# Kernel optimization log

Hardware: AMD Instinct MI355X
Metric: run time of the kernel (lower is better)

The kernel has to match this reference:

```python
import jax, jax.numpy as jnp
import numpy as np

B, S, H = 2, 2048, 4096
NH, NKV, HD = 32, 8, 128
ROPE_THETA = 10000.0


def setup_inputs() -> dict:
    key = jax.random.key(0)
    ks = jax.random.split(key, 5)
    hidden_states = jax.random.normal(ks[0], (B, S, H), dtype=jnp.float32)
    position_ids = jnp.tile(jnp.arange(S, dtype=jnp.int64)[None, :], (B, 1))
    Wq = jax.random.normal(ks[1], (H, NH * HD), dtype=jnp.float32) * 0.02
    Wk = jax.random.normal(ks[2], (H, NKV * HD), dtype=jnp.float32) * 0.02
    Wv = jax.random.normal(ks[3], (H, NKV * HD), dtype=jnp.float32) * 0.02
    Wo = jax.random.normal(ks[4], (NH * HD, H), dtype=jnp.float32) * 0.02
    return {"hidden_states": hidden_states, "position_ids": position_ids,
            "Wq": Wq, "Wk": Wk, "Wv": Wv, "Wo": Wo}


def _rotate_half(x):
    d = x.shape[-1] // 2
    return jnp.concatenate([-x[..., d:], x[..., :d]], axis=-1)


def reference(hidden_states, position_ids, Wq, Wk, Wv, Wo):
    b, s, _ = hidden_states.shape
    # QKV projections (no bias)
    q = (hidden_states @ Wq).reshape(b, s, NH, HD).transpose(0, 2, 1, 3)   # [b,nh,s,hd]
    k = (hidden_states @ Wk).reshape(b, s, NKV, HD).transpose(0, 2, 1, 3)  # [b,nkv,s,hd]
    v = (hidden_states @ Wv).reshape(b, s, NKV, HD).transpose(0, 2, 1, 3)
    # RoPE: cos/sin from cached table == analytic computation at position_ids
    inv_freq = 1.0 / (ROPE_THETA ** (jnp.arange(0, HD, 2, dtype=jnp.float32) / HD))
    freqs = position_ids.astype(jnp.float32)[:, :, None] * inv_freq  # [b,s,hd/2]
    emb = jnp.concatenate([freqs, freqs], axis=-1)                   # [b,s,hd]
    cos = jnp.cos(emb)[:, None, :, :]  # unsqueeze_dim=1 -> [b,1,s,hd]
    sin = jnp.sin(emb)[:, None, :, :]
    q = q * cos + _rotate_half(q) * sin
    k = k * cos + _rotate_half(k) * sin
    # GQA: repeat kv heads to match query heads
    groups = NH // NKV
    k = jnp.repeat(k, groups, axis=1)
    v = jnp.repeat(v, groups, axis=1)
    # causal SDPA
    scale = 1.0 / jnp.sqrt(jnp.float32(HD))
    scores = jnp.einsum('bhqd,bhkd->bhqk', q, k) * scale
    causal = jnp.tril(jnp.ones((s, s), dtype=bool))
    scores = jnp.where(causal[None, None], scores, jnp.finfo(scores.dtype).min)
    attn = jax.nn.softmax(scores, axis=-1)
    out = jnp.einsum('bhqk,bhkd->bhqd', attn, v)
    out = out.transpose(0, 2, 1, 3).reshape(b, s, NH * HD)
    return out @ Wo
```

## Files before the change

### kernel.cpp

```cpp
#include <hip/hip_runtime.h>
#include <cstdint>
#include <cstddef>

typedef unsigned short u16;
typedef unsigned int u32;
typedef short short8 __attribute__((ext_vector_type(8)));
typedef float f32x4 __attribute__((ext_vector_type(4)));

__device__ __forceinline__ u16 f2bf(float f) {
  unsigned u = __float_as_uint(f);
  u += 0x7fffu + ((u >> 16) & 1u);
  return (u16)(u >> 16);
}
__device__ __forceinline__ float bf2f(u16 h) {
  return __uint_as_float(((unsigned)h) << 16);
}
__device__ __forceinline__ u32 pack_bf2(float lo, float hi) {
  return ((u32)f2bf(hi) << 16) | (u32)f2bf(lo);
}

typedef const __attribute__((address_space(1))) unsigned int gu32_t;
typedef __attribute__((address_space(3))) unsigned int su32_t;
__device__ __forceinline__ void gl2lds16(const void* g, void* l) {
  __builtin_amdgcn_global_load_lds((gu32_t*)g, (su32_t*)l, 16, 0, 0);
}

__device__ __forceinline__ f32x4 mfma_bf16(short8 a, short8 b, f32x4 c) {
  return __builtin_amdgcn_mfma_f32_16x16x32_bf16(a, b, c, 0, 0, 0);
}

__global__ __launch_bounds__(256) void f32_to_bf16_kernel(
    const float* __restrict__ x, u16* __restrict__ y, int n) {
  int i = (blockIdx.x * 256 + threadIdx.x) * 4;
  if (i + 3 < n) {
    float4 v = *(const float4*)(x + i);
    ushort4 o;
    o.x = f2bf(v.x); o.y = f2bf(v.y); o.z = f2bf(v.z); o.w = f2bf(v.w);
    *(ushort4*)(y + i) = o;
  }
}

__global__ __launch_bounds__(256) void transpose_w_kernel(
    const float* __restrict__ W, u16* __restrict__ Wt, int K, int N) {
  __shared__ float tile[32][33];
  int n0 = blockIdx.x * 32, k0 = blockIdx.y * 32;
  int tx = threadIdx.x, ty = threadIdx.y;
#pragma unroll
  for (int j = 0; j < 4; ++j)
    tile[ty + j * 8][tx] = W[(size_t)(k0 + ty + j * 8) * N + n0 + tx];
  __syncthreads();
#pragma unroll
  for (int j = 0; j < 4; ++j)
    Wt[(size_t)(n0 + ty + j * 8) * K + k0 + tx] = f2bf(tile[tx][ty + j * 8]);
}

template <bool BF16OUT>
__global__ __launch_bounds__(256) void gemm_bt(
    const u16* __restrict__ A, const u16* __restrict__ Bt,
    float* __restrict__ Cf, u16* __restrict__ Cb, int K, int ldc) {
  __shared__ alignas(16) u16 As[128 * 32];
  __shared__ alignas(16) u16 Bs[128 * 32];
  const int tid = threadIdx.x;
  const int w = tid >> 6, lane = tid & 63;
  const int lq = lane & 15, qd = lane >> 4;
  const int wm = w >> 1, wn = w & 1;
  const int m0 = blockIdx.y * 128, n0 = blockIdx.x * 128;
  const int r4 = lane >> 2;
  const int csw = (((lane & 3) ^ ((lane >> 3) & 3)) * 8);
  const int sa = (lq >> 1) & 3;

  f32x4 acc[4][4] = {};

  const u16* ap = A + ((size_t)(m0 + w * 16 + r4) * K + csw);
  const u16* bp = Bt + ((size_t)(n0 + w * 16 + r4) * K + csw);
  u16* asd0 = &As[(w * 16) * 32];
  u16* asd1 = &As[(64 + w * 16) * 32];
  u16* bsd0 = &Bs[(w * 16) * 32];
  u16* bsd1 = &Bs[(64 + w * 16) * 32];

  for (int k0 = 0; k0 < K; k0 += 32) {
    gl2lds16(ap + k0, asd0);
    gl2lds16(ap + (size_t)64 * K + k0, asd1);
    gl2lds16(bp + k0, bsd0);
    gl2lds16(bp + (size_t)64 * K + k0, bsd1);
    __syncthreads();
    short8 af[4], bf[4];
#pragma unroll
    for (int i = 0; i < 4; ++i)
      af[i] = *(const short8*)&As[(wm * 64 + i * 16 + lq) * 32 + (qd ^ sa) * 8];
#pragma unroll
    for (int j = 0; j < 4; ++j)
      bf[j] = *(const short8*)&Bs[(wn * 64 + j * 16 + lq) * 32 + (qd ^ sa) * 8];
#pragma unroll
    for (int i = 0; i < 4; ++i)
#pragma unroll
      for (int j = 0; j < 4; ++j)
        acc[i][j] = mfma_bf16(af[i], bf[j], acc[i][j]);
    __syncthreads();
  }

#pragma unroll
  for (int i = 0; i < 4; ++i) {
    const int row = m0 + wm * 64 + i * 16 + qd * 4;
#pragma unroll
    for (int j = 0; j < 4; ++j) {
      const int col = n0 + wn * 64 + j * 16 + lq;
#pragma unroll
      for (int r = 0; r < 4; ++r) {
        if (BF16OUT)
          Cb[(size_t)(row + r) * ldc + col] = f2bf(acc[i][j][r]);
        else
          Cf[(size_t)(row + r) * ldc + col] = acc[i][j][r];
      }
    }
  }
}

__global__ __launch_bounds__(256) void rope_kernel(
    const u16* __restrict__ src, u16* __restrict__ dst,
    const int* __restrict__ pos_ids, int nh, int src_col0, int dst_ld, int total,
    float scale) {
  int idx = blockIdx.x * 256 + threadIdx.x;
  if (idx >= total) return;
  int i = idx & 63;
  int t = idx >> 6;
  int hh = t % nh;
  int m = t / nh;
  float pos = (float)pos_ids[m];
  float inv = exp2f(-(float)i * 0.20762050593046016f);
  float f = pos * inv;
  float c = cosf(f) * scale, s = sinf(f) * scale;
  const u16* sp = src + (size_t)m * 6144 + src_col0 + hh * 128;
  float x0 = bf2f(sp[i]);
  float x1 = bf2f(sp[i + 64]);
  u16* dp = dst + (size_t)m * dst_ld + hh * 128;
  dp[i] = f2bf(x0 * c - x1 * s);
  dp[i + 64] = f2bf(x1 * c + x0 * s);
}

__global__ __launch_bounds__(256) void vt_kernel(
    const u16* __restrict__ src, u16* __restrict__ vt) {
  __shared__ u16 tile[32][33];
  int s0 = blockIdx.x * 32;
  int d0 = blockIdx.y * 32;
  int bz = blockIdx.z;
  int b = bz >> 3, kvh = bz & 7;
  int tx = threadIdx.x, ty = threadIdx.y;
#pragma unroll
  for (int j = 0; j < 4; ++j)
    tile[ty + j * 8][tx] =
        src[(size_t)(b * 2048 + s0 + ty + j * 8) * 6144 + 5120 + kvh * 128 + d0 + tx];
  __syncthreads();
#pragma unroll
  for (int j = 0; j < 4; ++j)
    vt[((size_t)(b * 8 + kvh) * 128 + d0 + ty + j * 8) * 2048 + s0 + tx] =
        tile[tx][ty + j * 8];
}

#define PS_LD 76
__global__ __launch_bounds__(256, 3) void flash_kernel(
    const u16* __restrict__ Q, const u16* __restrict__ K,
    const u16* __restrict__ Vt, u16* __restrict__ O) {
  __shared__ alignas(16) u16 Ks[64 * 128];
  __shared__ alignas(16) u16 Vs[128 * 64];
  __shared__ alignas(16) u16 Ps[4][32 * PS_LD];

  const int tid = threadIdx.x;
  const int w = tid >> 6, lane = tid & 63;
  const int lq = lane & 15, qd = lane >> 4;
  const int lq7 = lq & 7;
  const int bh = blockIdx.y;
  const int b = bh >> 5, h = bh & 31, kvh = h >> 2;
  const int q0 = (gridDim.x - 1 - blockIdx.x) * 128;

  short8 qf[2][4];
  {
    const u16* qp = Q + ((size_t)(b * 2048 + q0 + w * 32 + lq) * 4096 + h * 128 + qd * 8);
#pragma unroll
    for (int n = 0; n < 2; ++n)
#pragma unroll
      for (int ks = 0; ks < 4; ++ks)
        qf[n][ks] = *(const short8*)(qp + (size_t)n * 16 * 4096 + ks * 32);
  }

  f32x4 ot[2][8] = {};
  float mprev[2], lsum[2];
#pragma unroll
  for (int n = 0; n < 2; ++n) { mprev[n] = -1e30f; lsum[n] = 0.f; }

  const int rk = lane >> 4;
  const int pk = lane & 15;
  const int ckA = (pk ^ rk) * 8;
  const int ckB = (pk ^ (4 + rk)) * 8;
  const int rv = lane >> 3;
  const int cv = ((lane & 7) ^ rv) * 8;

  const int kv_end = q0 + 128;

  for (int kv0 = 0; kv0 < kv_end; kv0 += 64) {
    {
      const u16* kbase = K + ((size_t)(b * 2048 + kv0 + w * 16 + rk) * 1024) + kvh * 128;
#pragma unroll
      for (int i = 0; i < 4; ++i)
        gl2lds16(kbase + (size_t)(i * 4) * 1024 + ((i & 1) ? ckB : ckA),
                 &Ks[(w * 16 + i * 4) * 128]);
      const u16* vbase = Vt + ((size_t)((b * 8 + kvh) * 128 + w * 32 + rv) * 2048) + kv0 + cv;
#pragma unroll
      for (int i = 0; i < 4; ++i)
        gl2lds16(vbase + (size_t)(i * 8) * 2048, &Vs[(w * 32 + i * 8) * 64]);
    }
    __syncthreads();

    f32x4 st[4][2] = {};
#pragma unroll
    for (int ks = 0; ks < 4; ++ks) {
      short8 kf[4];
#pragma unroll
      for (int m = 0; m < 4; ++m)
        kf[m] = *(const short8*)&Ks[(m * 16 + lq) * 128 + ((ks * 4 + qd) ^ lq7) * 8];
#pragma unroll
      for (int m = 0; m < 4; ++m)
#pragma unroll
        for (int n = 0; n < 2; ++n)
          st[m][n] = mfma_bf16(kf[m], qf[n][ks], st[m][n]);
    }

    if (kv0 + 63 > q0) {
#pragma unroll
      for (int n = 0; n < 2; ++n) {
        const int qrow = q0 + w * 32 + n * 16 + lq;
#pragma unroll
        for (int m = 0; m < 4; ++m) {
          const int kvb = kv0 + m * 16 + qd * 4;
#pragma unroll
          for (int r = 0; r < 4; ++r)
            if (kvb + r > qrow) st[m][n][r] = -1e30f;
        }
      }
    }

#pragma unroll
    for (int n = 0; n < 2; ++n) {
      float t = st[0][n][0];
#pragma unroll
      for (int m = 0; m < 4; ++m)
#pragma unroll
        for (int r = 0; r < 4; ++r) t = fmaxf(t, st[m][n][r]);
      t = fmaxf(t, __shfl_xor(t, 16));
      t = fmaxf(t, __shfl_xor(t, 32));
      const float mnew = fmaxf(mprev[n], t);
      const float alpha = __expf(mprev[n] - mnew);
      mprev[n] = mnew;

      float rs = 0.f;
      u32 pk2[4][2];
#pragma unroll
      for (int m = 0; m < 4; ++m) {
        float p0 = __expf(st[m][n][0] - mnew);
        float p1 = __expf(st[m][n][1] - mnew);
        float p2 = __expf(st[m][n][2] - mnew);
        float p3 = __expf(st[m][n][3] - mnew);
        rs += (p0 + p1) + (p2 + p3);
        pk2[m][0] = pack_bf2(p0, p1);
        pk2[m][1] = pack_bf2(p2, p3);
      }
      rs += __shfl_xor(rs, 16);
      rs += __shfl_xor(rs, 32);
      lsum[n] = lsum[n] * alpha + rs;

      u16* pw = &Ps[w][(n * 16 + lq) * PS_LD + qd * 4];
#pragma unroll
      for (int m = 0; m < 4; ++m)
        *(uint2*)(pw + m * 16) = make_uint2(pk2[m][0], pk2[m][1]);

#pragma unroll
      for (int mt = 0; mt < 8; ++mt)
#pragma unroll
        for (int r = 0; r < 4; ++r) ot[n][mt][r] *= alpha;
    }

#pragma unroll
    for (int kst = 0; kst < 2; ++kst) {
      short8 bp[2];
#pragma unroll
      for (int n = 0; n < 2; ++n)
        bp[n] = *(const short8*)&Ps[w][(n * 16 + lq) * PS_LD + kst * 32 + qd * 8];
#pragma unroll
      for (int mt = 0; mt < 8; ++mt) {
        short8 av = *(const short8*)&Vs[(mt * 16 + lq) * 64 + ((kst * 4 + qd) ^ lq7) * 8];
#pragma unroll
        for (int n = 0; n < 2; ++n)
          ot[n][mt] = mfma_bf16(av, bp[n], ot[n][mt]);
      }
    }
    __syncthreads();
  }

#pragma unroll
  for (int n = 0; n < 2; ++n) {
    const float inv = 1.f / lsum[n];
    const size_t row = (size_t)(b * 2048 + q0 + w * 32 + n * 16 + lq);
    u16* op = O + row * 4096 + h * 128 + qd * 4;
#pragma unroll
    for (int mt = 0; mt < 8; ++mt) {
      u32 a = pack_bf2(ot[n][mt][0] * inv, ot[n][mt][1] * inv);
      u32 c = pack_bf2(ot[n][mt][2] * inv, ot[n][mt][3] * inv);
      *(uint2*)(op + mt * 16) = make_uint2(a, c);
    }
  }
}

extern "C" void kernel_launch(void* const* d_in, const int* in_sizes, int n_in,
                              void* d_out, int out_size, void* d_ws, size_t ws_size,
                              hipStream_t stream) {
  const float* hidden = (const float*)d_in[0];
  const int* pos = (const int*)d_in[1];
  const float* Wq = (const float*)d_in[2];
  const float* Wk = (const float*)d_in[3];
  const float* Wv = (const float*)d_in[4];
  const float* Wo = (const float*)d_in[5];
  float* out = (float*)d_out;

  char* ws = (char*)d_ws;
  u16* hbf   = (u16*)(ws);
  u16* wqkvt = (u16*)(ws + 33554432ull);
  u16* wot   = (u16*)(ws + 83886080ull);
  u16* qkvbf = (u16*)(ws + 117440512ull);
  u16* qbf   = (u16*)(ws + 167772160ull);
  u16* kbf   = (u16*)(ws + 201326592ull);
  u16* vt    = (u16*)(ws + 209715200ull);
  u16* obf   = (u16*)(ws + 218103808ull);

  f32_to_bf16_kernel<<<16384, 256, 0, stream>>>(hidden, hbf, 16777216);
  transpose_w_kernel<<<dim3(128, 128), dim3(32, 8), 0, stream>>>(Wq, wqkvt, 4096, 4096);
  transpose_w_kernel<<<dim3(32, 128), dim3(32, 8), 0, stream>>>(Wk, wqkvt + (size_t)4096 * 4096, 4096, 1024);
  transpose_w_kernel<<<dim3(32, 128), dim3(32, 8), 0, stream>>>(Wv, wqkvt + (size_t)5120 * 4096, 4096, 1024);
  transpose_w_kernel<<<dim3(128, 128), dim3(32, 8), 0, stream>>>(Wo, wot, 4096, 4096);

  gemm_bt<true><<<dim3(48, 32), 256, 0, stream>>>(hbf, wqkvt, nullptr, qkvbf, 4096, 6144);

  rope_kernel<<<32768, 256, 0, stream>>>(qkvbf, qbf, pos, 32, 0, 4096, 8388608, 0.08838834764831845f);
  rope_kernel<<<8192, 256, 0, stream>>>(qkvbf, kbf, pos, 8, 4096, 1024, 2097152, 1.0f);

  vt_kernel<<<dim3(64, 4, 16), dim3(32, 8), 0, stream>>>(qkvbf, vt);

  flash_kernel<<<dim3(16, 64), 256, 0, stream>>>(qbf, kbf, vt, obf);

  gemm_bt<false><<<dim3(32, 32), 256, 0, stream>>>(obf, wot, out, nullptr, 4096, 4096);
}
```

Before: 1.012 ms.

## Make flash attention single-wave per block, reading K/V directly from global

Replaces the 4-wave block with cooperative LDS staging of K/V tiles by one-wave blocks of 32 query rows that load K and V fragments directly from global memory. This removes LDS staging and block-wide barriers and quadruples the grid size. In exchange, K/V reuse across query rows within a block is lost, raising L2/global traffic, and the strided per-lane loads are poorly coalesced.

```diff
diff --git a/kernel.cpp b/kernel.cpp
--- a/kernel.cpp
+++ b/kernel.cpp
@@ -158,24 +158,20 @@
 }
 
 #define PS_LD 76
-__global__ __launch_bounds__(256, 3) void flash_kernel(
+__global__ __launch_bounds__(64, 3) void flash_kernel(
     const u16* __restrict__ Q, const u16* __restrict__ K,
     const u16* __restrict__ Vt, u16* __restrict__ O) {
-  __shared__ alignas(16) u16 Ks[64 * 128];
-  __shared__ alignas(16) u16 Vs[128 * 64];
-  __shared__ alignas(16) u16 Ps[4][32 * PS_LD];
-
-  const int tid = threadIdx.x;
-  const int w = tid >> 6, lane = tid & 63;
+  __shared__ alignas(16) u16 Ps[32 * PS_LD];
+
+  const int lane = threadIdx.x;
   const int lq = lane & 15, qd = lane >> 4;
-  const int lq7 = lq & 7;
   const int bh = blockIdx.y;
   const int b = bh >> 5, h = bh & 31, kvh = h >> 2;
-  const int q0 = (gridDim.x - 1 - blockIdx.x) * 128;
+  const int qbase = (gridDim.x - 1 - blockIdx.x) * 32;
 
   short8 qf[2][4];
   {
-    const u16* qp = Q + ((size_t)(b * 2048 + q0 + w * 32 + lq) * 4096 + h * 128 + qd * 8);
+    const u16* qp = Q + ((size_t)(b * 2048 + qbase + lq) * 4096 + h * 128 + qd * 8);
 #pragma unroll
     for (int n = 0; n < 2; ++n)
 #pragma unroll
@@ -188,28 +184,13 @@
 #pragma unroll
   for (int n = 0; n < 2; ++n) { mprev[n] = -1e30f; lsum[n] = 0.f; }
 
-  const int rk = lane >> 4;
-  const int pk = lane & 15;
-  const int ckA = (pk ^ rk) * 8;
-  const int ckB = (pk ^ (4 + rk)) * 8;
-  const int rv = lane >> 3;
-  const int cv = ((lane & 7) ^ rv) * 8;
-
-  const int kv_end = q0 + 128;
-
-  for (int kv0 = 0; kv0 < kv_end; kv0 += 64) {
-    {
-      const u16* kbase = K + ((size_t)(b * 2048 + kv0 + w * 16 + rk) * 1024) + kvh * 128;
-#pragma unroll
-      for (int i = 0; i < 4; ++i)
-        gl2lds16(kbase + (size_t)(i * 4) * 1024 + ((i & 1) ? ckB : ckA),
-                 &Ks[(w * 16 + i * 4) * 128]);
-      const u16* vbase = Vt + ((size_t)((b * 8 + kvh) * 128 + w * 32 + rv) * 2048) + kv0 + cv;
-#pragma unroll
-      for (int i = 0; i < 4; ++i)
-        gl2lds16(vbase + (size_t)(i * 8) * 2048, &Vs[(w * 32 + i * 8) * 64]);
-    }
-    __syncthreads();
+  const u16* kp = K + ((size_t)(b * 2048 + lq) * 1024) + kvh * 128 + qd * 8;
+  const u16* vp = Vt + ((size_t)((b * 8 + kvh) * 128 + lq) * 2048) + qd * 8;
+
+  const int kv_iters = (qbase + 32 + 63) >> 6;
+
+  for (int it = 0; it < kv_iters; ++it) {
+    const int kv0 = it * 64;
 
     f32x4 st[4][2] = {};
 #pragma unroll
@@ -217,7 +198,7 @@
       short8 kf[4];
 #pragma unroll
       for (int m = 0; m < 4; ++m)
-        kf[m] = *(const short8*)&Ks[(m * 16 + lq) * 128 + ((ks * 4 + qd) ^ lq7) * 8];
+        kf[m] = *(const short8*)(kp + (size_t)(kv0 + m * 16) * 1024 + ks * 32);
 #pragma unroll
       for (int m = 0; m < 4; ++m)
 #pragma unroll
@@ -225,10 +206,10 @@
           st[m][n] = mfma_bf16(kf[m], qf[n][ks], st[m][n]);
     }
 
-    if (kv0 + 63 > q0) {
+    if (kv0 + 63 > qbase) {
 #pragma unroll
       for (int n = 0; n < 2; ++n) {
-        const int qrow = q0 + w * 32 + n * 16 + lq;
+        const int qrow = qbase + n * 16 + lq;
 #pragma unroll
         for (int m = 0; m < 4; ++m) {
           const int kvb = kv0 + m * 16 + qd * 4;
@@ -268,7 +249,7 @@
       rs += __shfl_xor(rs, 32);
       lsum[n] = lsum[n] * alpha + rs;
 
-      u16* pw = &Ps[w][(n * 16 + lq) * PS_LD + qd * 4];
+      u16* pw = &Ps[(n * 16 + lq) * PS_LD + qd * 4];
 #pragma unroll
       for (int m = 0; m < 4; ++m)
         *(uint2*)(pw + m * 16) = make_uint2(pk2[m][0], pk2[m][1]);
@@ -284,22 +265,21 @@
       short8 bp[2];
 #pragma unroll
       for (int n = 0; n < 2; ++n)
-        bp[n] = *(const short8*)&Ps[w][(n * 16 + lq) * PS_LD + kst * 32 + qd * 8];
+        bp[n] = *(const short8*)&Ps[(n * 16 + lq) * PS_LD + kst * 32 + qd * 8];
 #pragma unroll
       for (int mt = 0; mt < 8; ++mt) {
-        short8 av = *(const short8*)&Vs[(mt * 16 + lq) * 64 + ((kst * 4 + qd) ^ lq7) * 8];
+        short8 av = *(const short8*)(vp + (size_t)(mt * 16) * 2048 + kv0 + kst * 32);
 #pragma unroll
         for (int n = 0; n < 2; ++n)
           ot[n][mt] = mfma_bf16(av, bp[n], ot[n][mt]);
       }
     }
-    __syncthreads();
   }
 
 #pragma unroll
   for (int n = 0; n < 2; ++n) {
     const float inv = 1.f / lsum[n];
-    const size_t row = (size_t)(b * 2048 + q0 + w * 32 + n * 16 + lq);
+    const size_t row = (size_t)(b * 2048 + qbase + n * 16 + lq);
     u16* op = O + row * 4096 + h * 128 + qd * 4;
 #pragma unroll
     for (int mt = 0; mt < 8; ++mt) {
@@ -344,7 +324,7 @@
 
   vt_kernel<<<dim3(64, 4, 16), dim3(32, 8), 0, stream>>>(qkvbf, vt);
 
-  flash_kernel<<<dim3(16, 64), 256, 0, stream>>>(qbf, kbf, vt, obf);
+  flash_kernel<<<dim3(64, 64), 64, 0, stream>>>(qbf, kbf, vt, obf);
 
   gemm_bt<false><<<dim3(32, 32), 256, 0, stream>>>(obf, wot, out, nullptr, 4096, 4096);
 }
```

Result: slower. 1.193 ms (+17.9%).
